# Kernel tuning notes

Measured on AMD Instinct MI355X. Metric: run time of the kernel, lower is better.

## Reference

```python
import jax, jax.numpy as jnp
import numpy as np

B, T, D = 2, 2048, 1024
N_HEADS = 16
HEAD_DIM = D // N_HEADS


def setup_inputs() -> dict:
    key = jax.random.key(0)
    ks = jax.random.split(key, 5)
    s = 0.02
    return {
        "x": jax.random.normal(ks[0], (B, T, D), jnp.float32),
        "wq": jax.random.normal(ks[1], (D, D), jnp.float32) * s,
        "wk": jax.random.normal(ks[2], (D, D), jnp.float32) * s,
        "wv": jax.random.normal(ks[3], (D, D), jnp.float32) * s,
        "wo": jax.random.normal(ks[4], (D, D), jnp.float32) * s,
        "bo": jnp.zeros((D,), jnp.float32),
    }


def reference(x, wq, wk, wv, wo, bo):
    b, t, _ = x.shape
    # QKV projections (weights stored [d_in, d_out]); reshape to (b, heads, t, head_dim)
    def split_heads(y):
        return y.reshape(b, t, N_HEADS, HEAD_DIM).transpose(0, 2, 1, 3)
    q = split_heads(x @ wq)
    k = split_heads(x @ wk)
    v = split_heads(x @ wv)
    # causal attention scores: (b, h, t, t)
    scores = jnp.einsum("bhqd,bhkd->bhqk", q, k)
    causal = jnp.tril(jnp.ones((t, t), bool))  # True where attending allowed
    scores = jnp.where(causal, scores, -jnp.inf)
    attn = jax.nn.softmax(scores / np.sqrt(HEAD_DIM).astype(np.float32), axis=-1)
    # dropout_rate = 0.0 (eval mode) -> identity
    ctx = jnp.einsum("bhqk,bhkd->bhqd", attn, v)
    ctx = ctx.transpose(0, 2, 1, 3).reshape(b, t, D)
    return ctx @ wo + bo
```

## Files before the change

### kernel.cpp

```cpp
#include <hip/hip_runtime.h>
#include <hip/hip_bf16.h>
#include <cstdint>

typedef __hip_bfloat16 bf16;
typedef __bf16 bf16x8 __attribute__((ext_vector_type(8)));
typedef __bf16 bf16x4 __attribute__((ext_vector_type(4)));
typedef float f32x4 __attribute__((ext_vector_type(4)));

#define LOG2E 1.4426950408889634f

__device__ __forceinline__ void gload_lds16(const void* g, void* l) {
  __builtin_amdgcn_global_load_lds(
      (const __attribute__((address_space(1))) unsigned int*)g,
      (__attribute__((address_space(3))) unsigned int*)l,
      16, 0, 0);
}

__global__ void conv_k(const float* __restrict__ src, bf16* __restrict__ dst, int n) {
  const int i = (blockIdx.x * 256 + threadIdx.x) * 8;
  if (i >= n) return;
  const f32x4 a = *(const f32x4*)(src + i);
  const f32x4 b = *(const f32x4*)(src + i + 4);
  bf16x8 o;
#pragma unroll
  for (int j = 0; j < 4; ++j) { o[j] = (__bf16)a[j]; o[4 + j] = (__bf16)b[j]; }
  *(bf16x8*)(dst + i) = o;
}

__global__ void transpose_conv4(
    const float* __restrict__ wq, const float* __restrict__ wk,
    const float* __restrict__ wv, const float* __restrict__ wo,
    bf16* __restrict__ dqkv, bf16* __restrict__ dout) {
  __shared__ float tile[32][33];
  const int z = blockIdx.z;
  const float* src = (z == 0) ? wq : ((z == 1) ? wk : ((z == 2) ? wv : wo));
  bf16* dst = (z < 3) ? (dqkv + (long)z * 1048576) : dout;
  const int bx = blockIdx.x * 32, by = blockIdx.y * 32;
  const int tx = threadIdx.x;
  for (int j = threadIdx.y; j < 32; j += 8)
    tile[j][tx] = src[(long)(by + j) * 1024 + bx + tx];
  __syncthreads();
  for (int j = threadIdx.y; j < 32; j += 8)
    dst[(long)(bx + j) * 1024 + by + tx] = __float2bfloat16(tile[tx][j]);
}

__global__ __launch_bounds__(256, 2) void gemm_qkv(
    const bf16* __restrict__ A, const bf16* __restrict__ Bt,
    bf16* __restrict__ Cq, bf16* __restrict__ Ck, bf16* __restrict__ Cv,
    int M, int N, int K) {
  __shared__ __align__(16) bf16 As[128 * 32];
  __shared__ __align__(16) bf16 Bs[128 * 32];

  const int tid = threadIdx.x;
  const int lane = tid & 63;
  const int wave = tid >> 6;
  const int quad = lane >> 4;
  const int l16 = lane & 15;
  const int m0 = blockIdx.y * 128;
  const int n0 = blockIdx.x * 128;
  const int wm = (wave >> 1) * 64;
  const int wn = (wave & 1) * 64;

  const f32x4 zero4 = {0.f, 0.f, 0.f, 0.f};
  f32x4 acc[4][4];
#pragma unroll
  for (int mi = 0; mi < 4; ++mi)
#pragma unroll
    for (int ni = 0; ni < 4; ++ni) acc[mi][ni] = zero4;

  const int sRow = tid >> 2;
  const int sK = (tid & 3) * 8;
  const bf16* Ag = A + (long)(m0 + sRow) * K + sK;
  const bf16* Ag2 = Ag + 64L * K;
  const bf16* Bg = Bt + (long)(n0 + sRow) * K + sK;
  const bf16* Bg2 = Bg + 64L * K;

  for (int k0 = 0; k0 < K; k0 += 32) {
    gload_lds16(Ag + k0, &As[tid * 8]);
    gload_lds16(Ag2 + k0, &As[tid * 8 + 2048]);
    gload_lds16(Bg + k0, &Bs[tid * 8]);
    gload_lds16(Bg2 + k0, &Bs[tid * 8 + 2048]);
    __syncthreads();

    bf16x8 af[4], bfv[4];
#pragma unroll
    for (int mi = 0; mi < 4; ++mi)
      af[mi] = *(const bf16x8*)&As[(wm + mi * 16 + l16) * 32 + quad * 8];
#pragma unroll
    for (int ni = 0; ni < 4; ++ni)
      bfv[ni] = *(const bf16x8*)&Bs[(wn + ni * 16 + l16) * 32 + quad * 8];
#pragma unroll
    for (int mi = 0; mi < 4; ++mi)
#pragma unroll
      for (int ni = 0; ni < 4; ++ni)
        acc[mi][ni] = __builtin_amdgcn_mfma_f32_16x16x32_bf16(af[mi], bfv[ni], acc[mi][ni], 0, 0, 0);
    __syncthreads();
  }

#pragma unroll
  for (int mi = 0; mi < 4; ++mi) {
    const int gmb = m0 + wm + mi * 16 + quad * 4;
#pragma unroll
    for (int ni = 0; ni < 4; ++ni) {
      const int n = n0 + wn + ni * 16 + l16;
      const int which = n >> 10, rem = n & 1023;
      const int h = rem >> 6, hd = rem & 63;
      bf16* dst = (which == 0) ? Cq : ((which == 1) ? Ck : Cv);
#pragma unroll
      for (int r = 0; r < 4; ++r) {
        const int gm = gmb + r;
        const int b = gm >> 11, t = gm & 2047;
        dst[(((long)(b * 16 + h)) * 2048 + t) * 64 + hd] = __float2bfloat16(acc[mi][ni][r]);
      }
    }
  }
}

__global__ __launch_bounds__(256, 4) void gemm_out(
    const bf16* __restrict__ A, const bf16* __restrict__ Bt,
    const float* __restrict__ bias, float* __restrict__ Cout,
    int M, int N, int K) {
  __shared__ __align__(16) bf16 As[64 * 32];
  __shared__ __align__(16) bf16 Bs[128 * 32];

  const int tid = threadIdx.x;
  const int lane = tid & 63;
  const int wave = tid >> 6;
  const int quad = lane >> 4;
  const int l16 = lane & 15;
  const int m0 = blockIdx.y * 64;
  const int n0 = blockIdx.x * 128;
  const int wm = (wave & 1) * 32;
  const int wn = (wave >> 1) * 64;

  const f32x4 zero4 = {0.f, 0.f, 0.f, 0.f};
  f32x4 acc[2][4];
#pragma unroll
  for (int mi = 0; mi < 2; ++mi)
#pragma unroll
    for (int ni = 0; ni < 4; ++ni) acc[mi][ni] = zero4;

  const int sRow = tid >> 2;
  const int sK = (tid & 3) * 8;
  const bf16* Ag = A + (long)(m0 + sRow) * K + sK;
  const bf16* Bg = Bt + (long)(n0 + sRow) * K + sK;
  const bf16* Bg2 = Bg + 64L * K;

  for (int k0 = 0; k0 < K; k0 += 32) {
    gload_lds16(Ag + k0, &As[tid * 8]);
    gload_lds16(Bg + k0, &Bs[tid * 8]);
    gload_lds16(Bg2 + k0, &Bs[tid * 8 + 2048]);
    __syncthreads();

    bf16x8 af[2], bfv[4];
#pragma unroll
    for (int mi = 0; mi < 2; ++mi)
      af[mi] = *(const bf16x8*)&As[(wm + mi * 16 + l16) * 32 + quad * 8];
#pragma unroll
    for (int ni = 0; ni < 4; ++ni)
      bfv[ni] = *(const bf16x8*)&Bs[(wn + ni * 16 + l16) * 32 + quad * 8];
#pragma unroll
    for (int mi = 0; mi < 2; ++mi)
#pragma unroll
      for (int ni = 0; ni < 4; ++ni)
        acc[mi][ni] = __builtin_amdgcn_mfma_f32_16x16x32_bf16(af[mi], bfv[ni], acc[mi][ni], 0, 0, 0);
    __syncthreads();
  }

#pragma unroll
  for (int mi = 0; mi < 2; ++mi) {
    const int gmb = m0 + wm + mi * 16 + quad * 4;
#pragma unroll
    for (int ni = 0; ni < 4; ++ni) {
      const int n = n0 + wn + ni * 16 + l16;
      const float bv = bias[n];
#pragma unroll
      for (int r = 0; r < 4; ++r)
        Cout[(long)(gmb + r) * N + n] = acc[mi][ni][r] + bv;
    }
  }
}

__global__ __launch_bounds__(256, 4) void attn_kernel(
    const bf16* __restrict__ Q, const bf16* __restrict__ Kg, const bf16* __restrict__ Vg,
    bf16* __restrict__ ctx) {
  constexpr int KSTR = 72, VSTR = 136;
  __shared__ __align__(16) bf16 Ks[128 * KSTR];
  __shared__ __align__(16) bf16 Vt[64 * VSTR];

  const int tid = threadIdx.x;
  const int lane = tid & 63;
  const int wave = tid >> 6;
  const int quad = lane >> 4;
  const int l16 = lane & 15;

  const int x = blockIdx.x;
  const int s4 = blockIdx.y >> 3;
  int qt;
  if (s4 == 0)      qt = x;
  else if (s4 == 1) qt = 31 - x;
  else if (s4 == 2) qt = x ^ 16;
  else              qt = 31 - (x ^ 16);

  const int bh = blockIdx.y;
  const long base = (long)bh * 2048 * 64;
  const int qbase = qt * 64 + wave * 16;
  const int q = qbase + l16;

  const bf16x8 qf0 = *(const bf16x8*)(Q + base + (long)(qbase + l16) * 64 + quad * 8);
  const bf16x8 qf1 = *(const bf16x8*)(Q + base + (long)(qbase + l16) * 64 + 32 + quad * 8);

  const f32x4 zero4 = {0.f, 0.f, 0.f, 0.f};
  float m_i = -1e30f, l_i = 0.f;
  f32x4 oacc[4];
#pragma unroll
  for (int nb = 0; nb < 4; ++nb) oacc[nb] = zero4;

  const int krow = tid >> 1;
  const int kc32 = (tid & 1) * 32;
  const int vr4 = (tid & 31) * 4;
  const int vd8 = (tid >> 5) * 8;

  const int nk = (qt + 2) >> 1;
  bf16x8 kr[4], vv[4];
  {
    const bf16* kp = Kg + base + (long)krow * 64 + kc32;
#pragma unroll
    for (int i = 0; i < 4; ++i) kr[i] = *(const bf16x8*)(kp + i * 8);
#pragma unroll
    for (int i = 0; i < 4; ++i)
      vv[i] = *(const bf16x8*)(Vg + base + (long)(vr4 + i) * 64 + vd8);
  }

  for (int kt = 0; kt < nk; ++kt) {
    const int k0 = kt * 128;
#pragma unroll
    for (int i = 0; i < 4; ++i)
      *(bf16x8*)&Ks[krow * KSTR + kc32 + i * 8] = kr[i];
#pragma unroll
    for (int j = 0; j < 8; ++j) {
      bf16x4 t;
      t[0] = vv[0][j]; t[1] = vv[1][j]; t[2] = vv[2][j]; t[3] = vv[3][j];
      *(bf16x4*)&Vt[(vd8 + j) * VSTR + vr4] = t;
    }
    __syncthreads();
    if (kt + 1 < nk) {
      const bf16* kp = Kg + base + (long)(k0 + 128 + krow) * 64 + kc32;
#pragma unroll
      for (int i = 0; i < 4; ++i) kr[i] = *(const bf16x8*)(kp + i * 8);
#pragma unroll
      for (int i = 0; i < 4; ++i)
        vv[i] = *(const bf16x8*)(Vg + base + (long)(k0 + 128 + vr4 + i) * 64 + vd8);
    }

    f32x4 s[8];
#pragma unroll
    for (int kb = 0; kb < 8; ++kb) {
      const bf16x8 kb0 = *(const bf16x8*)&Ks[(kb * 16 + l16) * KSTR + quad * 8];
      const bf16x8 kb1 = *(const bf16x8*)&Ks[(kb * 16 + l16) * KSTR + 32 + quad * 8];
      f32x4 a = zero4;
      a = __builtin_amdgcn_mfma_f32_16x16x32_bf16(kb0, qf0, a, 0, 0, 0);
      a = __builtin_amdgcn_mfma_f32_16x16x32_bf16(kb1, qf1, a, 0, 0, 0);
      s[kb] = a;
    }

    float mloc = -1e30f;
#pragma unroll
    for (int kb = 0; kb < 8; ++kb) {
#pragma unroll
      for (int r = 0; r < 4; ++r) {
        const int kidx = k0 + kb * 16 + quad * 4 + r;
        float sv = s[kb][r] * 0.125f;
        sv = (kidx <= q) ? sv : -1e30f;
        s[kb][r] = sv;
        mloc = fmaxf(mloc, sv);
      }
    }
    mloc = fmaxf(mloc, __shfl_xor(mloc, 16));
    mloc = fmaxf(mloc, __shfl_xor(mloc, 32));

    const float mn = fmaxf(m_i, mloc);
    const float alpha = exp2f((m_i - mn) * LOG2E);
    float rsum = 0.f;
    uint32_t pkw[8][2];
#pragma unroll
    for (int kb = 0; kb < 8; ++kb) {
      const float p0 = exp2f((s[kb][0] - mn) * LOG2E);
      const float p1 = exp2f((s[kb][1] - mn) * LOG2E);
      const float p2 = exp2f((s[kb][2] - mn) * LOG2E);
      const float p3 = exp2f((s[kb][3] - mn) * LOG2E);
      rsum += (p0 + p1) + (p2 + p3);
      union { __bf16 h[2]; uint32_t u; } ua, ub;
      ua.h[0] = (__bf16)p0; ua.h[1] = (__bf16)p1;
      ub.h[0] = (__bf16)p2; ub.h[1] = (__bf16)p3;
      pkw[kb][0] = ua.u; pkw[kb][1] = ub.u;
    }
    rsum += __shfl_xor(rsum, 16);
    rsum += __shfl_xor(rsum, 32);
    l_i = l_i * alpha + rsum;
    m_i = mn;

    float alr[4];
#pragma unroll
    for (int r = 0; r < 4; ++r) alr[r] = __shfl(alpha, quad * 4 + r);
#pragma unroll
    for (int nb = 0; nb < 4; ++nb)
#pragma unroll
      for (int r = 0; r < 4; ++r) oacc[nb][r] *= alr[r];

    bf16x8 pa[4];
#pragma unroll
    for (int kk = 0; kk < 4; ++kk) {
      const uint32_t lo0 = pkw[2 * kk][0],     lo1 = pkw[2 * kk][1];
      const uint32_t hi0 = pkw[2 * kk + 1][0], hi1 = pkw[2 * kk + 1][1];
      const uint32_t v16a = (quad < 2) ? lo0 : hi0, v16b = (quad < 2) ? lo1 : hi1;
      const uint32_t v32a = (quad == 0) ? hi0 : lo0, v32b = (quad == 0) ? hi1 : lo1;
      const uint32_t v48a = (quad == 1) ? hi0 : lo0, v48b = (quad == 1) ? hi1 : lo1;
      const uint32_t x16a = __shfl_xor(v16a, 16), x16b = __shfl_xor(v16b, 16);
      const uint32_t x32a = __shfl_xor(v32a, 32), x32b = __shfl_xor(v32b, 32);
      const uint32_t x48a = __shfl_xor(v48a, 48), x48b = __shfl_xor(v48b, 48);
      uint32_t w0, w1, w2, w3;
      if (quad == 0)      { w0 = lo0;  w1 = lo1;  w2 = x16a; w3 = x16b; }
      else if (quad == 1) { w0 = x48a; w1 = x48b; w2 = x32a; w3 = x32b; }
      else if (quad == 2) { w0 = x32a; w1 = x32b; w2 = x48a; w3 = x48b; }
      else                { w0 = x16a; w1 = x16b; w2 = hi0;  w3 = hi1; }
      union { uint32_t u[4]; bf16x8 v; } pu;
      pu.u[0] = w0; pu.u[1] = w1; pu.u[2] = w2; pu.u[3] = w3;
      pa[kk] = pu.v;
    }

#pragma unroll
    for (int nb2 = 0; nb2 < 4; ++nb2) {
#pragma unroll
      for (int kk = 0; kk < 4; ++kk) {
        const bf16x8 vb = *(const bf16x8*)&Vt[(nb2 * 16 + l16) * VSTR + kk * 32 + quad * 8];
        oacc[nb2] = __builtin_amdgcn_mfma_f32_16x16x32_bf16(pa[kk], vb, oacc[nb2], 0, 0, 0);
      }
    }
    __syncthreads();
  }

  const int b = bh >> 4, h = bh & 15;
  float linv[4];
#pragma unroll
  for (int r = 0; r < 4; ++r) linv[r] = 1.0f / __shfl(l_i, quad * 4 + r);
#pragma unroll
  for (int r = 0; r < 4; ++r) {
    const int t = qbase + quad * 4 + r;
#pragma unroll
    for (int nb2 = 0; nb2 < 4; ++nb2) {
      const int d = h * 64 + nb2 * 16 + l16;
      ctx[((long)b * 2048 + t) * 1024 + d] = __float2bfloat16(oacc[nb2][r] * linv[r]);
    }
  }
}

extern "C" void kernel_launch(void* const* d_in, const int* in_sizes, int n_in,
                              void* d_out, int out_size, void* d_ws, size_t ws_size,
                              hipStream_t stream) {
  const float* x  = (const float*)d_in[0];
  const float* wq = (const float*)d_in[1];
  const float* wk = (const float*)d_in[2];
  const float* wv = (const float*)d_in[3];
  const float* wo = (const float*)d_in[4];
  const float* bo = (const float*)d_in[5];
  float* out = (float*)d_out;

  bf16* Wtqkv = (bf16*)d_ws;
  bf16* Wto   = Wtqkv + 3145728;
  bf16* xb    = Wto + 1048576;
  bf16* Qb    = xb + 4194304;
  bf16* Kb    = Qb + 4194304;
  bf16* Vb    = Kb + 4194304;
  bf16* Cx    = xb;

  hipLaunchKernelGGL(conv_k, dim3(2048), dim3(256), 0, stream, x, xb, 4194304);
  hipLaunchKernelGGL(transpose_conv4, dim3(32, 32, 4), dim3(32, 8), 0, stream,
                     wq, wk, wv, wo, Wtqkv, Wto);

  hipLaunchKernelGGL(gemm_qkv, dim3(24, 32), dim3(256), 0, stream,
                     xb, Wtqkv, Qb, Kb, Vb, 4096, 3072, 1024);

  hipLaunchKernelGGL(attn_kernel, dim3(32, 32), dim3(256), 0, stream, Qb, Kb, Vb, Cx);

  hipLaunchKernelGGL(gemm_out, dim3(8, 64), dim3(256), 0, stream,
                     Cx, Wto, bo, out, 4096, 1024, 1024);
}
```

Before: 211.5 us.

## Streamline flash-attention softmax: prescale Q, lazy rescale, mask only diagonal tile

Folds the 1/sqrt(d) scale into Q once at load, and applies the causal mask only on the last (diagonal) key tile. Rescaling of the accumulator is skipped when the running max grows by 8 or less, and the exponent becomes a single fma with a precomputed offset. The P-to-A-operand shuffle is replaced by one xor-16 exchange, paired with a permuted V-fragment read of two 4-element halves so the k ordering still matches. This cuts VALU and cross-lane work in the softmax, at the cost of Q rounding after scaling, possible exp values up to 2^8 before normalization, and split LDS reads for V.

Measured after the change: 248.2 us. 17.3% more time.

```diff
diff --git a/kernel.cpp b/kernel.cpp
--- a/kernel.cpp
+++ b/kernel.cpp
@@ -207,11 +207,16 @@
   const int qbase = qt * 64 + wave * 16;
   const int q = qbase + l16;
 
-  const bf16x8 qf0 = *(const bf16x8*)(Q + base + (long)(qbase + l16) * 64 + quad * 8);
-  const bf16x8 qf1 = *(const bf16x8*)(Q + base + (long)(qbase + l16) * 64 + 32 + quad * 8);
+  bf16x8 qf0 = *(const bf16x8*)(Q + base + (long)(qbase + l16) * 64 + quad * 8);
+  bf16x8 qf1 = *(const bf16x8*)(Q + base + (long)(qbase + l16) * 64 + 32 + quad * 8);
+#pragma unroll
+  for (int j = 0; j < 8; ++j) {
+    qf0[j] = (__bf16)((float)qf0[j] * 0.125f);
+    qf1[j] = (__bf16)((float)qf1[j] * 0.125f);
+  }
 
   const f32x4 zero4 = {0.f, 0.f, 0.f, 0.f};
-  float m_i = -1e30f, l_i = 0.f;
+  float m_i = -1e30f, l_i = 0.f, negml = 0.f;
   f32x4 oacc[4];
 #pragma unroll
   for (int nb = 0; nb < 4; ++nb) oacc[nb] = zero4;
@@ -220,6 +225,8 @@
   const int kc32 = (tid & 1) * 32;
   const int vr4 = (tid & 31) * 4;
   const int vd8 = (tid >> 5) * 8;
+  const int vq0 = quad * 4;
+  const int vq1 = 16 + (quad ^ 1) * 4;
 
   const int nk = (qt + 2) >> 1;
   bf16x8 kr[4], vv[4];
@@ -264,77 +271,85 @@
       s[kb] = a;
     }
 
-    float mloc = -1e30f;
-#pragma unroll
-    for (int kb = 0; kb < 8; ++kb) {
-#pragma unroll
-      for (int r = 0; r < 4; ++r) {
-        const int kidx = k0 + kb * 16 + quad * 4 + r;
-        float sv = s[kb][r] * 0.125f;
-        sv = (kidx <= q) ? sv : -1e30f;
-        s[kb][r] = sv;
-        mloc = fmaxf(mloc, sv);
+    float mloc;
+    if (kt == nk - 1) {
+      const int qg = q - k0 - quad * 4;
+      mloc = -1e30f;
+#pragma unroll
+      for (int kb = 0; kb < 8; ++kb) {
+#pragma unroll
+        for (int r = 0; r < 4; ++r) {
+          float sv = (kb * 16 + r <= qg) ? s[kb][r] : -1e30f;
+          s[kb][r] = sv;
+          mloc = fmaxf(mloc, sv);
+        }
       }
+    } else {
+      float mk[8];
+#pragma unroll
+      for (int kb = 0; kb < 8; ++kb)
+        mk[kb] = fmaxf(fmaxf(s[kb][0], s[kb][1]), fmaxf(s[kb][2], s[kb][3]));
+      mloc = fmaxf(fmaxf(fmaxf(mk[0], mk[1]), fmaxf(mk[2], mk[3])),
+                   fmaxf(fmaxf(mk[4], mk[5]), fmaxf(mk[6], mk[7])));
     }
     mloc = fmaxf(mloc, __shfl_xor(mloc, 16));
     mloc = fmaxf(mloc, __shfl_xor(mloc, 32));
 
-    const float mn = fmaxf(m_i, mloc);
-    const float alpha = exp2f((m_i - mn) * LOG2E);
-    float rsum = 0.f;
+    if (!__all(mloc <= m_i + 8.f)) {
+      const float mn = fmaxf(m_i, mloc);
+      const float alpha = exp2f((m_i - mn) * LOG2E);
+      float alr[4];
+#pragma unroll
+      for (int r = 0; r < 4; ++r) alr[r] = __shfl(alpha, quad * 4 + r);
+#pragma unroll
+      for (int nb = 0; nb < 4; ++nb)
+#pragma unroll
+        for (int r = 0; r < 4; ++r) oacc[nb][r] *= alr[r];
+      l_i *= alpha;
+      m_i = mn;
+      negml = -mn * LOG2E;
+    }
+
+    float rs0 = 0.f, rs1 = 0.f;
     uint32_t pkw[8][2];
 #pragma unroll
     for (int kb = 0; kb < 8; ++kb) {
-      const float p0 = exp2f((s[kb][0] - mn) * LOG2E);
-      const float p1 = exp2f((s[kb][1] - mn) * LOG2E);
-      const float p2 = exp2f((s[kb][2] - mn) * LOG2E);
-      const float p3 = exp2f((s[kb][3] - mn) * LOG2E);
-      rsum += (p0 + p1) + (p2 + p3);
+      const float p0 = exp2f(fmaf(s[kb][0], LOG2E, negml));
+      const float p1 = exp2f(fmaf(s[kb][1], LOG2E, negml));
+      const float p2 = exp2f(fmaf(s[kb][2], LOG2E, negml));
+      const float p3 = exp2f(fmaf(s[kb][3], LOG2E, negml));
+      rs0 += p0 + p1;
+      rs1 += p2 + p3;
       union { __bf16 h[2]; uint32_t u; } ua, ub;
       ua.h[0] = (__bf16)p0; ua.h[1] = (__bf16)p1;
       ub.h[0] = (__bf16)p2; ub.h[1] = (__bf16)p3;
       pkw[kb][0] = ua.u; pkw[kb][1] = ub.u;
     }
+    float rsum = rs0 + rs1;
     rsum += __shfl_xor(rsum, 16);
     rsum += __shfl_xor(rsum, 32);
-    l_i = l_i * alpha + rsum;
-    m_i = mn;
-
-    float alr[4];
-#pragma unroll
-    for (int r = 0; r < 4; ++r) alr[r] = __shfl(alpha, quad * 4 + r);
-#pragma unroll
-    for (int nb = 0; nb < 4; ++nb)
-#pragma unroll
-      for (int r = 0; r < 4; ++r) oacc[nb][r] *= alr[r];
+    l_i += rsum;
 
     bf16x8 pa[4];
 #pragma unroll
     for (int kk = 0; kk < 4; ++kk) {
-      const uint32_t lo0 = pkw[2 * kk][0],     lo1 = pkw[2 * kk][1];
-      const uint32_t hi0 = pkw[2 * kk + 1][0], hi1 = pkw[2 * kk + 1][1];
-      const uint32_t v16a = (quad < 2) ? lo0 : hi0, v16b = (quad < 2) ? lo1 : hi1;
-      const uint32_t v32a = (quad == 0) ? hi0 : lo0, v32b = (quad == 0) ? hi1 : lo1;
-      const uint32_t v48a = (quad == 1) ? hi0 : lo0, v48b = (quad == 1) ? hi1 : lo1;
-      const uint32_t x16a = __shfl_xor(v16a, 16), x16b = __shfl_xor(v16b, 16);
-      const uint32_t x32a = __shfl_xor(v32a, 32), x32b = __shfl_xor(v32b, 32);
-      const uint32_t x48a = __shfl_xor(v48a, 48), x48b = __shfl_xor(v48b, 48);
-      uint32_t w0, w1, w2, w3;
-      if (quad == 0)      { w0 = lo0;  w1 = lo1;  w2 = x16a; w3 = x16b; }
-      else if (quad == 1) { w0 = x48a; w1 = x48b; w2 = x32a; w3 = x32b; }
-      else if (quad == 2) { w0 = x32a; w1 = x32b; w2 = x48a; w3 = x48b; }
-      else                { w0 = x16a; w1 = x16b; w2 = hi0;  w3 = hi1; }
       union { uint32_t u[4]; bf16x8 v; } pu;
-      pu.u[0] = w0; pu.u[1] = w1; pu.u[2] = w2; pu.u[3] = w3;
+      pu.u[0] = pkw[2 * kk][0];
+      pu.u[1] = pkw[2 * kk][1];
+      pu.u[2] = (uint32_t)__shfl_xor((int)pkw[2 * kk + 1][0], 16);
+      pu.u[3] = (uint32_t)__shfl_xor((int)pkw[2 * kk + 1][1], 16);
       pa[kk] = pu.v;
     }
 
 #pragma unroll
     for (int nb2 = 0; nb2 < 4; ++nb2) {
+      const int vrow = (nb2 * 16 + l16) * VSTR;
 #pragma unroll
       for (int kk = 0; kk < 4; ++kk) {
-        const bf16x8 vb = *(const bf16x8*)&Vt[(nb2 * 16 + l16) * VSTR + kk * 32 + quad * 8];
-        oacc[nb2] = __builtin_amdgcn_mfma_f32_16x16x32_bf16(pa[kk], vb, oacc[nb2], 0, 0, 0);
+        union { bf16x4 h[2]; bf16x8 v; } vu;
+        vu.h[0] = *(const bf16x4*)&Vt[vrow + kk * 32 + vq0];
+        vu.h[1] = *(const bf16x4*)&Vt[vrow + kk * 32 + vq1];
+        oacc[nb2] = __builtin_amdgcn_mfma_f32_16x16x32_bf16(pa[kk], vu.v, oacc[nb2], 0, 0, 0);
       }
     }
     __syncthreads();
```
